# Performance work log

Hardware: AMD Instinct MI355X
Metric: run time of the kernel (lower is better)

## Reference

```python
import jax, jax.numpy as jnp
import numpy as np

B, T, D = 2, 2048, 1024
H, RANK = 16, 16
HD = D // H  # 64


def setup_inputs() -> dict:
    key = jax.random.key(0)
    ks = jax.random.split(key, 10)
    x = jax.random.normal(ks[0], (B, T, D), dtype=jnp.float32)
    def lin(k):
        kw, kb = jax.random.split(k)
        W = jax.random.normal(kw, (D, D), dtype=jnp.float32) * (1.0 / np.sqrt(D))
        b = jax.random.normal(kb, (D,), dtype=jnp.float32) * 0.01
        return W, b
    Wq, bq = lin(ks[1])
    Wk, bk = lin(ks[2])
    Wv, bv = lin(ks[3])
    Wo, bo = lin(ks[4])
    # per-head low-rank metric factors A_h: (min(rank, head_dim), head_dim)
    A = jax.random.normal(ks[5], (H, min(RANK, HD), HD), dtype=jnp.float32) * 0.02
    log_lambda = jnp.full((H,), jnp.log(jnp.float32(0.1)), dtype=jnp.float32)
    return {"x": x, "Wq": Wq, "bq": bq, "Wk": Wk, "bk": bk,
            "Wv": Wv, "bv": bv, "Wo": Wo, "bo": bo,
            "A": A, "log_lambda": log_lambda}


def reference(x, Wq, bq, Wk, bk, Wv, bv, Wo, bo, A, log_lambda):
    b, t, d = x.shape
    h = A.shape[0]
    hd = d // h

    def split_heads(y):
        return y.reshape(b, t, h, hd).transpose(0, 2, 1, 3)  # (b,h,t,hd)

    q = split_heads(x @ Wq.T + bq)
    k = split_heads(x @ Wk.T + bk)
    v = split_heads(x @ Wv.T + bv)

    # Metric g_h = A_h^T A_h + lam_h * I. torch.einsum('btid,dd,btjd->btj')
    # uses only diag(g) and sums over i: dist[b,t,j] = sum_d S[b,t,d]*gdiag[d]*diff[b,t,j,d]
    # where S[b,t,d] = sum_i (q[b,t,d] - k[b,i,d]) = t*q - sum_i k.
    gdiag = jnp.sum(A * A, axis=1) + jnp.exp(log_lambda)[:, None]  # (h,hd)

    ksum = jnp.sum(k, axis=2)                      # (b,h,hd)
    S = jnp.float32(t) * q - ksum[:, :, None, :]   # (b,h,t,hd)
    Sg = S * gdiag[None, :, None, :]               # (b,h,t,hd)
    c = jnp.sum(Sg * q, axis=-1)                   # (b,h,t)
    # dist_sq[b,h,t,j] = c[b,h,t] - sum_d Sg[b,h,t,d] * k[b,h,j,d]
    dist_sq = c[..., None] - jnp.einsum('bhtd,bhjd->bhtj', Sg, k)
    attn = jax.nn.softmax(-dist_sq, axis=-1)       # (b,h,t,t)
    o = jnp.einsum('bhtj,bhjd->bhtd', attn, v)     # (b,h,t,hd)
    out = o.transpose(0, 2, 1, 3).reshape(b, t, d)
    return out @ Wo.T + bo
```

## Files before the change

kernel.cpp:

```cpp
#include <hip/hip_runtime.h>
#include <math.h>

#define D_MODEL 1024
#define NHEAD   16
#define HDIM    64
#define SEQ     2048
#define BATCH   2
#define NROWS   (BATCH*SEQ)

typedef unsigned short u16;
typedef __attribute__((ext_vector_type(4))) unsigned short u16x4;
typedef __attribute__((ext_vector_type(8))) short short8;
typedef __attribute__((ext_vector_type(4))) float f32x4;
typedef __attribute__((ext_vector_type(2))) unsigned int u32x2;

#define SWZ(row, c) (((c) ^ ((row) & 7)) * 8)
#define GF(row) ((((row) + ((row) >> 2))) & 3)

__device__ __forceinline__ u16 f2bf(float x) {
    unsigned int u = __float_as_uint(x);
    u += 0x7fffu + ((u >> 16) & 1u);
    return (u16)(u >> 16);
}
__device__ __forceinline__ float bf2f(u16 h) {
    return __uint_as_float(((unsigned int)h) << 16);
}
__device__ __forceinline__ unsigned int cvt_pk_bf16(float a, float b) {
    unsigned int r;
    asm("v_cvt_pk_bf16_f32 %0, %1, %2" : "=v"(r) : "v"(a), "v"(b));
    return r;
}
__device__ __forceinline__ void st8(u16* p, short8 v) {
    u16x4 a, b;
    a[0]=(u16)v[0]; a[1]=(u16)v[1]; a[2]=(u16)v[2]; a[3]=(u16)v[3];
    b[0]=(u16)v[4]; b[1]=(u16)v[5]; b[2]=(u16)v[6]; b[3]=(u16)v[7];
    *(u16x4*)p = a; *(u16x4*)(p + 4) = b;
}
__device__ __forceinline__ void gld16(const u16* g, u16* l) {
    __builtin_amdgcn_global_load_lds(
        (const __attribute__((address_space(1))) void*)g,
        (__attribute__((address_space(3))) void*)l, 16, 0, 0);
}

__device__ __forceinline__ void xcd_decode(int bid, int& member, int& g) {
    const int xcd = bid & 7;
    const int rest = bid >> 3;
    member = rest & 15;
    g = ((rest >> 4) << 3) | xcd;
}

__global__ void gdiag_kernel(const float* __restrict__ A,
                             const float* __restrict__ log_lambda,
                             float* __restrict__ gdiag) {
    int id = blockIdx.x * 256 + threadIdx.x;
    if (id >= NHEAD * HDIM) return;
    int h = id >> 6, d = id & 63;
    float s = 0.f;
#pragma unroll
    for (int i = 0; i < 16; ++i) {
        float a = A[(h * 16 + i) * HDIM + d];
        s += a * a;
    }
    gdiag[id] = (s + __expf(log_lambda[h])) * 1.4426950408889634f;
}

__global__ void prep_split(const float* __restrict__ x,
                           const float* __restrict__ Wq, const float* __restrict__ Wk,
                           const float* __restrict__ Wv, const float* __restrict__ Wo,
                           u16* __restrict__ xh, u16* __restrict__ xl,
                           u16* __restrict__ wqh, u16* __restrict__ wql,
                           u16* __restrict__ wkh, u16* __restrict__ wkl,
                           u16* __restrict__ wvh, u16* __restrict__ woh) {
    int seg = blockIdx.y;
    int i = blockIdx.x * 256 + threadIdx.x;
    const float* src; u16* dh; u16* dl; int n4;
    if      (seg == 0) { src = x;  dh = xh;  dl = xl;      n4 = NROWS * D_MODEL / 4; }
    else if (seg == 1) { src = Wq; dh = wqh; dl = wql;     n4 = D_MODEL * D_MODEL / 4; }
    else if (seg == 2) { src = Wk; dh = wkh; dl = wkl;     n4 = D_MODEL * D_MODEL / 4; }
    else if (seg == 3) { src = Wv; dh = wvh; dl = nullptr; n4 = D_MODEL * D_MODEL / 4; }
    else               { src = Wo; dh = woh; dl = nullptr; n4 = D_MODEL * D_MODEL / 4; }
    if (i >= n4) return;
    float4 v = *(const float4*)&src[(size_t)i * 4];
    float vv[4] = {v.x, v.y, v.z, v.w};
    u16x4 hv, lv;
#pragma unroll
    for (int j = 0; j < 4; ++j) {
        u16 hb = f2bf(vv[j]);
        hv[j] = hb;
        lv[j] = f2bf(vv[j] - bf2f(hb));
    }
    *(u16x4*)&dh[(size_t)i * 4] = hv;
    if (dl) *(u16x4*)&dl[(size_t)i * 4] = lv;
}

template<int NP3>
__global__ __launch_bounds__(512, 4)
void gemm_mfma(const u16* __restrict__ Ah, const u16* __restrict__ Al,
               const u16* __restrict__ BhA, const u16* __restrict__ BlA, const float* __restrict__ biasA,
               float* outfA, u16* auxhA, u16* auxlA, float* ksumA,
               const u16* __restrict__ BhB, const u16* __restrict__ BlB, const float* __restrict__ biasB,
               float* outfB, u16* auxhB, u16* auxlB, float* ksumB,
               int out_layout) {
    int xtile, g;
    xcd_decode(blockIdx.x, xtile, g);
    const int ytile = g & 31;
    const int z = g >> 5;

    const u16* Bh = (z == 0) ? BhA : BhB;
    const u16* Bl = (z == 0) ? BlA : BlB;
    const float* bias = (z == 0) ? biasA : biasB;
    float* outf = (z == 0) ? outfA : outfB;
    u16* auxh   = (z == 0) ? auxhA : auxhB;
    u16* auxl   = (z == 0) ? auxlA : auxlB;
    float* ksump= (z == 0) ? ksumA : ksumB;

    __shared__ __align__(16) u16 As_h[128][32], Bs_h[64][32];
    __shared__ __align__(16) u16 As_l[NP3 ? 128 : 1][32], Bs_l[NP3 ? 64 : 1][32];

    const int tid = threadIdx.x;
    const int w = tid >> 6, lane = tid & 63, quad = lane >> 4, n16 = lane & 15;
    const int rBase = ytile * 128;
    const int cBase = xtile * 64;

    const int lrow = lane >> 2;
    const int lch  = lane & 3;
    const int arow = w * 16 + lrow;
    const int asc  = ((lch ^ GF(arow)) * 8);
    const int brow = (w & 3) * 16 + lrow;
    const int bsc  = ((lch ^ GF(brow)) * 8);

    f32x4 acc[4] = {};

    for (int kt = 0; kt < D_MODEL; kt += 32) {
        gld16(&Ah[(size_t)(rBase + arow) * D_MODEL + kt + asc], &As_h[w * 16][0]);
        if (NP3) gld16(&Al[(size_t)(rBase + arow) * D_MODEL + kt + asc], &As_l[w * 16][0]);
        if (w < 4) {
            gld16(&Bh[(size_t)(cBase + brow) * D_MODEL + kt + bsc], &Bs_h[(w & 3) * 16][0]);
        } else if (NP3) {
            gld16(&Bl[(size_t)(cBase + brow) * D_MODEL + kt + bsc], &Bs_l[NP3 ? (w & 3) * 16 : 0][0]);
        }
        __syncthreads();

        short8 a_h, a_l;
        {
            const int row = w * 16 + n16;
            const int cc = (quad ^ GF(row)) * 8;
            a_h = *(const short8*)&As_h[row][cc];
            if (NP3) a_l = *(const short8*)&As_l[NP3 ? row : 0][cc];
        }
#pragma unroll
        for (int nt = 0; nt < 4; ++nt) {
            const int row = nt * 16 + n16;
            const int cc = (quad ^ GF(row)) * 8;
            short8 b_h = *(const short8*)&Bs_h[row][cc];
            short8 b_l;
            if (NP3) b_l = *(const short8*)&Bs_l[NP3 ? row : 0][cc];
            acc[nt] = __builtin_amdgcn_mfma_f32_16x16x32_bf16(a_h, b_h, acc[nt], 0, 0, 0);
            if (NP3) {
                acc[nt] = __builtin_amdgcn_mfma_f32_16x16x32_bf16(a_h, b_l, acc[nt], 0, 0, 0);
                acc[nt] = __builtin_amdgcn_mfma_f32_16x16x32_bf16(a_l, b_h, acc[nt], 0, 0, 0);
            }
        }
        __syncthreads();
    }

    float csum[4];
#pragma unroll
    for (int nt = 0; nt < 4; ++nt) csum[nt] = 0.f;
#pragma unroll
    for (int nt = 0; nt < 4; ++nt) {
        int c = cBase + nt * 16 + n16;
        float bc = bias[c];
        int rb = rBase + w * 16 + quad * 4;
#pragma unroll
        for (int reg = 0; reg < 4; ++reg) {
            float val = acc[nt][reg] + bc;
            int rr = rb + reg;
            size_t idx = out_layout
                ? ((size_t)(((rr >> 11) * NHEAD + (c >> 6)) * SEQ + (rr & (SEQ - 1)))) * HDIM + (c & 63)
                : (size_t)rr * D_MODEL + c;
            if (outf) outf[idx] = val;
            if (auxh) {
                u16 hb = f2bf(val);
                auxh[idx] = hb;
                if (auxl) auxl[idx] = f2bf(val - bf2f(hb));
            }
            csum[nt] += val;
        }
    }
    if (ksump) {
#pragma unroll
        for (int nt = 0; nt < 4; ++nt) {
            float cs = csum[nt];
            cs += __shfl_xor(cs, 16);
            cs += __shfl_xor(cs, 32);
            if (quad == 0) {
                int c = cBase + nt * 16 + n16;
                int bb = rBase >> 11;
                atomicAdd(&ksump[(bb * NHEAD + (c >> 6)) * HDIM + (c & 63)], cs);
            }
        }
    }
}

__global__ __launch_bounds__(256)
void vtrans_kernel(const u16* __restrict__ vh, u16* __restrict__ vT) {
    __shared__ u16 tile[64][72];
    const int tid = threadIdx.x;
    const int t0 = blockIdx.x * 64;
    const int bh = blockIdx.y;
    const u16* vp = vh + (size_t)bh * SEQ * HDIM;
#pragma unroll
    for (int s = 0; s < 2; ++s) {
        int id = s * 256 + tid;
        int row = id >> 3, c8 = (id & 7) * 8;
        st8(&tile[row][c8], *(const short8*)&vp[(size_t)(t0 + row) * HDIM + c8]);
    }
    __syncthreads();
#pragma unroll
    for (int s = 0; s < 2; ++s) {
        int id = s * 256 + tid;
        int d = id >> 3, t8 = (id & 7) * 8;
        short8 r;
#pragma unroll
        for (int i = 0; i < 8; ++i) r[i] = (short)tile[t8 + i][d];
        *(short8*)&vT[((size_t)bh * HDIM + d) * SEQ + t0 + t8] = r;
    }
}

__global__ __launch_bounds__(256, 2)
void flash_mfma(const float* __restrict__ q, const u16* __restrict__ kh,
                const u16* __restrict__ kl, const u16* __restrict__ vT,
                const float* __restrict__ ksum, const float* __restrict__ gdiag,
                u16* __restrict__ o) {
    __shared__ __align__(16) u16 khs[2][64][64], kls[2][64][64], vTs[2][64][64];
    __shared__ __align__(16) u16 ps[4][32][64];

    const int tid = threadIdx.x;
    const int w = tid >> 6, lane = tid & 63, quad = lane >> 4, n16 = lane & 15;
    int qblk, g;
    xcd_decode(blockIdx.x, qblk, g);
    const int t0 = qblk * 128;
    const int h = g & 15, b = g >> 4;
    const size_t bh = (size_t)b * NHEAD + h;
    const float* qp = q + bh * SEQ * HDIM;
    const u16* khp = kh + bh * SEQ * HDIM;
    const u16* klp = kl + bh * SEQ * HDIM;
    const u16* vtp = vT + bh * HDIM * SEQ;

    short8 sgh[2][2], sgl[2][2];
#pragma unroll
    for (int mt = 0; mt < 2; ++mt) {
        int qrow = t0 + w * 32 + mt * 16 + n16;
#pragma unroll
        for (int kc = 0; kc < 2; ++kc) {
            int d0 = kc * 32 + quad * 8;
            float4 q0 = *(const float4*)&qp[(size_t)qrow * HDIM + d0];
            float4 q1 = *(const float4*)&qp[(size_t)qrow * HDIM + d0 + 4];
            float4 k0 = *(const float4*)&ksum[bh * HDIM + d0];
            float4 k1 = *(const float4*)&ksum[bh * HDIM + d0 + 4];
            float4 g0 = *(const float4*)&gdiag[(size_t)h * HDIM + d0];
            float4 g1 = *(const float4*)&gdiag[(size_t)h * HDIM + d0 + 4];
            float sg[8];
            sg[0] = (2048.f * q0.x - k0.x) * g0.x; sg[1] = (2048.f * q0.y - k0.y) * g0.y;
            sg[2] = (2048.f * q0.z - k0.z) * g0.z; sg[3] = (2048.f * q0.w - k0.w) * g0.w;
            sg[4] = (2048.f * q1.x - k1.x) * g1.x; sg[5] = (2048.f * q1.y - k1.y) * g1.y;
            sg[6] = (2048.f * q1.z - k1.z) * g1.z; sg[7] = (2048.f * q1.w - k1.w) * g1.w;
#pragma unroll
            for (int j = 0; j < 8; ++j) {
                u16 hb = f2bf(sg[j]);
                sgh[mt][kc][j] = (short)hb;
                sgl[mt][kc][j] = (short)f2bf(sg[j] - bf2f(hb));
            }
        }
    }

    f32x4 oaccv[2][4] = {};
    float m_n[2] = {-INFINITY, -INFINITY};
    float l_n[2] = {0.f, 0.f};

    const int srow = tid >> 3;
    const int sc   = tid & 7;
    const int scg  = sc * 8;
    const int scl  = SWZ(srow, sc);

    short8 rk0h = *(const short8*)&khp[(size_t)srow * HDIM + scg];
    short8 rk1h = *(const short8*)&khp[(size_t)(srow + 32) * HDIM + scg];
    short8 rk0l = *(const short8*)&klp[(size_t)srow * HDIM + scg];
    short8 rk1l = *(const short8*)&klp[(size_t)(srow + 32) * HDIM + scg];
    short8 rv0  = *(const short8*)&vtp[(size_t)srow * SEQ + scg];
    short8 rv1  = *(const short8*)&vtp[(size_t)(srow + 32) * SEQ + scg];
    *(short8*)&khs[0][srow][scl] = rk0h;  *(short8*)&khs[0][srow + 32][scl] = rk1h;
    *(short8*)&kls[0][srow][scl] = rk0l;  *(short8*)&kls[0][srow + 32][scl] = rk1l;
    *(short8*)&vTs[0][srow][scl] = rv0;   *(short8*)&vTs[0][srow + 32][scl] = rv1;

    int cur = 0;
    for (int j0 = 0; j0 < SEQ; j0 += 64, cur ^= 1) {
        __syncthreads();
        const int jn = j0 + 64;
        const bool pf = (jn < SEQ);
        if (pf) {
            rk0h = *(const short8*)&khp[(size_t)(jn + srow) * HDIM + scg];
            rk1h = *(const short8*)&khp[(size_t)(jn + srow + 32) * HDIM + scg];
            rk0l = *(const short8*)&klp[(size_t)(jn + srow) * HDIM + scg];
            rk1l = *(const short8*)&klp[(size_t)(jn + srow + 32) * HDIM + scg];
            rv0  = *(const short8*)&vtp[(size_t)srow * SEQ + jn + scg];
            rv1  = *(const short8*)&vtp[(size_t)(srow + 32) * SEQ + jn + scg];
        }

        f32x4 lgT[2][4] = {};
#pragma unroll
        for (int kc = 0; kc < 2; ++kc) {
#pragma unroll
            for (int nt = 0; nt < 4; ++nt) {
                const int row = nt * 16 + n16;
                const int cc = SWZ(row, kc * 4 + quad);
                short8 b_h = *(const short8*)&khs[cur][row][cc];
                short8 b_l = *(const short8*)&kls[cur][row][cc];
#pragma unroll
                for (int mt = 0; mt < 2; ++mt) {
                    lgT[mt][nt] = __builtin_amdgcn_mfma_f32_16x16x32_bf16(b_h, sgh[mt][kc], lgT[mt][nt], 0, 0, 0);
                    lgT[mt][nt] = __builtin_amdgcn_mfma_f32_16x16x32_bf16(b_l, sgh[mt][kc], lgT[mt][nt], 0, 0, 0);
                    lgT[mt][nt] = __builtin_amdgcn_mfma_f32_16x16x32_bf16(b_h, sgl[mt][kc], lgT[mt][nt], 0, 0, 0);
                }
            }
        }

        float mx[2];
#pragma unroll
        for (int mt = 0; mt < 2; ++mt) {
            float m0 = fmaxf(fmaxf(lgT[mt][0][0], lgT[mt][0][1]), lgT[mt][0][2]);
            m0 = fmaxf(fmaxf(m0, lgT[mt][0][3]), lgT[mt][1][0]);
            m0 = fmaxf(fmaxf(m0, lgT[mt][1][1]), lgT[mt][1][2]);
            m0 = fmaxf(fmaxf(m0, lgT[mt][1][3]), lgT[mt][2][0]);
            m0 = fmaxf(fmaxf(m0, lgT[mt][2][1]), lgT[mt][2][2]);
            m0 = fmaxf(fmaxf(m0, lgT[mt][2][3]), lgT[mt][3][0]);
            m0 = fmaxf(fmaxf(m0, lgT[mt][3][1]), lgT[mt][3][2]);
            m0 = fmaxf(m0, lgT[mt][3][3]);
            m0 = fmaxf(m0, __shfl_xor(m0, 16));
            mx[mt] = fmaxf(m0, __shfl_xor(m0, 32));
        }

        const float need = fmaxf(mx[0] - m_n[0], mx[1] - m_n[1]);
        if (!__all(need <= 8.f)) {
#pragma unroll
            for (int mt = 0; mt < 2; ++mt) {
                const float mn = fmaxf(m_n[mt], mx[mt]);
                const float alpha = exp2f(m_n[mt] - mn);
                m_n[mt] = mn;
                l_n[mt] *= alpha;
                const float a0 = __shfl(alpha, quad * 4 + 0);
                const float a1 = __shfl(alpha, quad * 4 + 1);
                const float a2 = __shfl(alpha, quad * 4 + 2);
                const float a3 = __shfl(alpha, quad * 4 + 3);
#pragma unroll
                for (int nt = 0; nt < 4; ++nt) {
                    oaccv[mt][nt][0] *= a0; oaccv[mt][nt][1] *= a1;
                    oaccv[mt][nt][2] *= a2; oaccv[mt][nt][3] *= a3;
                }
            }
        }

#pragma unroll
        for (int mt = 0; mt < 2; ++mt) {
            const int prow = mt * 16 + n16;
            const float mn = m_n[mt];
            float psum = 0.f;
#pragma unroll
            for (int nt = 0; nt < 4; ++nt) {
#pragma unroll
                for (int r = 0; r < 4; ++r) lgT[mt][nt][r] = exp2f(lgT[mt][nt][r] - mn);
                u32x2 pk;
                pk[0] = cvt_pk_bf16(lgT[mt][nt][0], lgT[mt][nt][1]);
                pk[1] = cvt_pk_bf16(lgT[mt][nt][2], lgT[mt][nt][3]);
                *(u32x2*)&ps[w][prow][SWZ(prow, nt * 2 + (quad >> 1)) + (quad & 1) * 4] = pk;
                psum += (lgT[mt][nt][0] + lgT[mt][nt][1]) + (lgT[mt][nt][2] + lgT[mt][nt][3]);
            }
            l_n[mt] += psum;
        }

        short8 pa[2][2];
#pragma unroll
        for (int mt = 0; mt < 2; ++mt) {
            const int prow = mt * 16 + n16;
            pa[mt][0] = *(const short8*)&ps[w][prow][SWZ(prow, quad)];
            pa[mt][1] = *(const short8*)&ps[w][prow][SWZ(prow, quad + 4)];
        }
#pragma unroll
        for (int nt = 0; nt < 4; ++nt) {
            const int row = nt * 16 + n16;
            short8 v0 = *(const short8*)&vTs[cur][row][SWZ(row, quad)];
            short8 v1 = *(const short8*)&vTs[cur][row][SWZ(row, quad + 4)];
#pragma unroll
            for (int mt = 0; mt < 2; ++mt) {
                oaccv[mt][nt] = __builtin_amdgcn_mfma_f32_16x16x32_bf16(pa[mt][0], v0, oaccv[mt][nt], 0, 0, 0);
                oaccv[mt][nt] = __builtin_amdgcn_mfma_f32_16x16x32_bf16(pa[mt][1], v1, oaccv[mt][nt], 0, 0, 0);
            }
        }

        if (pf) {
            const int nx = cur ^ 1;
            *(short8*)&khs[nx][srow][scl] = rk0h;  *(short8*)&khs[nx][srow + 32][scl] = rk1h;
            *(short8*)&kls[nx][srow][scl] = rk0l;  *(short8*)&kls[nx][srow + 32][scl] = rk1l;
            *(short8*)&vTs[nx][srow][scl] = rv0;   *(short8*)&vTs[nx][srow + 32][scl] = rv1;
        }
    }

#pragma unroll
    for (int mt = 0; mt < 2; ++mt) {
        float l = l_n[mt];
        l += __shfl_xor(l, 16);
        l += __shfl_xor(l, 32);
        l_n[mt] = l;
    }
#pragma unroll
    for (int mt = 0; mt < 2; ++mt) {
#pragma unroll
        for (int r = 0; r < 4; ++r) {
            float lr = __shfl(l_n[mt], quad * 4 + r);
            float inv = 1.f / lr;
            int t = t0 + w * 32 + mt * 16 + quad * 4 + r;
#pragma unroll
            for (int nt = 0; nt < 4; ++nt) {
                int d = nt * 16 + n16;
                o[((size_t)(b * SEQ + t)) * D_MODEL + h * HDIM + d] = f2bf(oaccv[mt][nt][r] * inv);
            }
        }
    }
}

extern "C" void kernel_launch(void* const* d_in, const int* in_sizes, int n_in,
                              void* d_out, int out_size, void* d_ws, size_t ws_size,
                              hipStream_t stream) {
    const float* x  = (const float*)d_in[0];
    const float* Wq = (const float*)d_in[1];
    const float* bq = (const float*)d_in[2];
    const float* Wk = (const float*)d_in[3];
    const float* bk = (const float*)d_in[4];
    const float* Wv = (const float*)d_in[5];
    const float* bv = (const float*)d_in[6];
    const float* Wo = (const float*)d_in[7];
    const float* bo = (const float*)d_in[8];
    const float* A  = (const float*)d_in[9];
    const float* ll = (const float*)d_in[10];
    float* out = (float*)d_out;

    const size_t NQKV = (size_t)NROWS * D_MODEL;
    const size_t NW = (size_t)D_MODEL * D_MODEL;
    char* base = (char*)d_ws;
    float* q_ws = (float*)base;            base += NQKV * 4;
    u16* xh  = (u16*)base;                 base += NQKV * 2;
    u16* xl  = (u16*)base;                 base += NQKV * 2;
    u16* khw = (u16*)base;                 base += NQKV * 2;
    u16* klw = (u16*)base;                 base += NQKV * 2;
    u16* vhw = (u16*)base;                 base += NQKV * 2;
    u16* wqh = (u16*)base;                 base += NW * 2;
    u16* wql = (u16*)base;                 base += NW * 2;
    u16* wkh = (u16*)base;                 base += NW * 2;
    u16* wkl = (u16*)base;                 base += NW * 2;
    u16* wvh = (u16*)base;                 base += NW * 2;
    u16* woh = (u16*)base;                 base += NW * 2;
    float* gd_ws   = (float*)base;         base += NHEAD * HDIM * 4;
    float* ksum_ws = (float*)base;         base += BATCH * NHEAD * HDIM * 4;

    hipMemsetAsync(ksum_ws, 0, BATCH * NHEAD * HDIM * sizeof(float), stream);

    prep_split<<<dim3(4096, 5), 256, 0, stream>>>(x, Wq, Wk, Wv, Wo,
                                                  xh, xl, wqh, wql, wkh, wkl, wvh, woh);
    gdiag_kernel<<<4, 256, 0, stream>>>(A, ll, gd_ws);

    gemm_mfma<1><<<1024, 512, 0, stream>>>(
        xh, xl,
        wqh, wql, bq, q_ws, nullptr, nullptr, nullptr,
        wkh, wkl, bk, nullptr, khw, klw, ksum_ws,
        1);
    gemm_mfma<0><<<512, 512, 0, stream>>>(
        xh, nullptr,
        wvh, nullptr, bv, nullptr, vhw, nullptr, nullptr,
        wvh, nullptr, bv, nullptr, vhw, nullptr, nullptr,
        1);

    u16* vTw = xl;
    u16* ohw = xh;
    vtrans_kernel<<<dim3(SEQ / 64, BATCH * NHEAD), 256, 0, stream>>>(vhw, vTw);

    flash_mfma<<<512, 256, 0, stream>>>(
        q_ws, khw, klw, vTw, ksum_ws, gd_ws, ohw);

    gemm_mfma<0><<<512, 512, 0, stream>>>(
        ohw, nullptr,
        woh, nullptr, bo, out, nullptr, nullptr, nullptr,
        woh, nullptr, bo, out, nullptr, nullptr, nullptr,
        0);
}
```

Baseline: 297.0 us.

## Software-pipeline QK MFMA of next tile with softmax/PV of previous tile

Restructures the flash attention loop so the QK^T MFMAs for tile j are issued alongside the softmax and PV for tile j-1, letting MFMA work overlap with exp and LDS traffic. V gets a triple-buffered LDS slot because it is consumed one iteration later than K. This costs more registers for the carried logits (lgP) and more LDS, which may put the two-blocks-per-CU occupancy target at risk or cause spills.

```diff
diff --git a/kernel.cpp b/kernel.cpp
--- a/kernel.cpp
+++ b/kernel.cpp
@@ -228,12 +228,113 @@
     }
 }
 
+__device__ __forceinline__ void qk_mfma(f32x4 (&lg)[2][4],
+                                        const u16 (*kh)[64], const u16 (*kl)[64],
+                                        const short8 (&sgh)[2][2], const short8 (&sgl)[2][2],
+                                        int quad, int n16) {
+#pragma unroll
+    for (int mt = 0; mt < 2; ++mt)
+#pragma unroll
+        for (int nt = 0; nt < 4; ++nt) lg[mt][nt] = (f32x4){0.f, 0.f, 0.f, 0.f};
+#pragma unroll
+    for (int kc = 0; kc < 2; ++kc) {
+#pragma unroll
+        for (int nt = 0; nt < 4; ++nt) {
+            const int row = nt * 16 + n16;
+            const int cc = SWZ(row, kc * 4 + quad);
+            short8 b_h = *(const short8*)&kh[row][cc];
+            short8 b_l = *(const short8*)&kl[row][cc];
+#pragma unroll
+            for (int mt = 0; mt < 2; ++mt) {
+                lg[mt][nt] = __builtin_amdgcn_mfma_f32_16x16x32_bf16(b_h, sgh[mt][kc], lg[mt][nt], 0, 0, 0);
+                lg[mt][nt] = __builtin_amdgcn_mfma_f32_16x16x32_bf16(b_l, sgh[mt][kc], lg[mt][nt], 0, 0, 0);
+                lg[mt][nt] = __builtin_amdgcn_mfma_f32_16x16x32_bf16(b_h, sgl[mt][kc], lg[mt][nt], 0, 0, 0);
+            }
+        }
+    }
+}
+
+__device__ __forceinline__ void softmax_pv(f32x4 (&lg)[2][4], float (&m_n)[2], float (&l_n)[2],
+                                           f32x4 (&oaccv)[2][4],
+                                           u16 (*psw)[64],
+                                           const u16 (*vt)[64],
+                                           int quad, int n16) {
+    float mx[2];
+#pragma unroll
+    for (int mt = 0; mt < 2; ++mt) {
+        float m0 = fmaxf(fmaxf(lg[mt][0][0], lg[mt][0][1]), lg[mt][0][2]);
+        m0 = fmaxf(fmaxf(m0, lg[mt][0][3]), lg[mt][1][0]);
+        m0 = fmaxf(fmaxf(m0, lg[mt][1][1]), lg[mt][1][2]);
+        m0 = fmaxf(fmaxf(m0, lg[mt][1][3]), lg[mt][2][0]);
+        m0 = fmaxf(fmaxf(m0, lg[mt][2][1]), lg[mt][2][2]);
+        m0 = fmaxf(fmaxf(m0, lg[mt][2][3]), lg[mt][3][0]);
+        m0 = fmaxf(fmaxf(m0, lg[mt][3][1]), lg[mt][3][2]);
+        m0 = fmaxf(m0, lg[mt][3][3]);
+        m0 = fmaxf(m0, __shfl_xor(m0, 16));
+        mx[mt] = fmaxf(m0, __shfl_xor(m0, 32));
+    }
+    const float need = fmaxf(mx[0] - m_n[0], mx[1] - m_n[1]);
+    if (!__all(need <= 8.f)) {
+#pragma unroll
+        for (int mt = 0; mt < 2; ++mt) {
+            const float mn = fmaxf(m_n[mt], mx[mt]);
+            const float alpha = exp2f(m_n[mt] - mn);
+            m_n[mt] = mn;
+            l_n[mt] *= alpha;
+            const float a0 = __shfl(alpha, quad * 4 + 0);
+            const float a1 = __shfl(alpha, quad * 4 + 1);
+            const float a2 = __shfl(alpha, quad * 4 + 2);
+            const float a3 = __shfl(alpha, quad * 4 + 3);
+#pragma unroll
+            for (int nt = 0; nt < 4; ++nt) {
+                oaccv[mt][nt][0] *= a0; oaccv[mt][nt][1] *= a1;
+                oaccv[mt][nt][2] *= a2; oaccv[mt][nt][3] *= a3;
+            }
+        }
+    }
+#pragma unroll
+    for (int mt = 0; mt < 2; ++mt) {
+        const int prow = mt * 16 + n16;
+        const float mn = m_n[mt];
+        float psum = 0.f;
+#pragma unroll
+        for (int nt = 0; nt < 4; ++nt) {
+#pragma unroll
+            for (int r = 0; r < 4; ++r) lg[mt][nt][r] = exp2f(lg[mt][nt][r] - mn);
+            u32x2 pk;
+            pk[0] = cvt_pk_bf16(lg[mt][nt][0], lg[mt][nt][1]);
+            pk[1] = cvt_pk_bf16(lg[mt][nt][2], lg[mt][nt][3]);
+            *(u32x2*)&psw[prow][SWZ(prow, nt * 2 + (quad >> 1)) + (quad & 1) * 4] = pk;
+            psum += (lg[mt][nt][0] + lg[mt][nt][1]) + (lg[mt][nt][2] + lg[mt][nt][3]);
+        }
+        l_n[mt] += psum;
+    }
+    short8 pa[2][2];
+#pragma unroll
+    for (int mt = 0; mt < 2; ++mt) {
+        const int prow = mt * 16 + n16;
+        pa[mt][0] = *(const short8*)&psw[prow][SWZ(prow, quad)];
+        pa[mt][1] = *(const short8*)&psw[prow][SWZ(prow, quad + 4)];
+    }
+#pragma unroll
+    for (int nt = 0; nt < 4; ++nt) {
+        const int row = nt * 16 + n16;
+        short8 v0 = *(const short8*)&vt[row][SWZ(row, quad)];
+        short8 v1 = *(const short8*)&vt[row][SWZ(row, quad + 4)];
+#pragma unroll
+        for (int mt = 0; mt < 2; ++mt) {
+            oaccv[mt][nt] = __builtin_amdgcn_mfma_f32_16x16x32_bf16(pa[mt][0], v0, oaccv[mt][nt], 0, 0, 0);
+            oaccv[mt][nt] = __builtin_amdgcn_mfma_f32_16x16x32_bf16(pa[mt][1], v1, oaccv[mt][nt], 0, 0, 0);
+        }
+    }
+}
+
 __global__ __launch_bounds__(256, 2)
 void flash_mfma(const float* __restrict__ q, const u16* __restrict__ kh,
                 const u16* __restrict__ kl, const u16* __restrict__ vT,
                 const float* __restrict__ ksum, const float* __restrict__ gdiag,
                 u16* __restrict__ o) {
-    __shared__ __align__(16) u16 khs[2][64][64], kls[2][64][64], vTs[2][64][64];
+    __shared__ __align__(16) u16 khs[2][64][64], kls[2][64][64], vTs[3][64][64];
     __shared__ __align__(16) u16 ps[4][32][64];
 
     const int tid = threadIdx.x;
@@ -276,6 +377,7 @@
     }
 
     f32x4 oaccv[2][4] = {};
+    f32x4 lgP[2][4];
     float m_n[2] = {-INFINITY, -INFINITY};
     float l_n[2] = {0.f, 0.f};
 
@@ -284,22 +386,36 @@
     const int scg  = sc * 8;
     const int scl  = SWZ(srow, sc);
 
-    short8 rk0h = *(const short8*)&khp[(size_t)srow * HDIM + scg];
-    short8 rk1h = *(const short8*)&khp[(size_t)(srow + 32) * HDIM + scg];
-    short8 rk0l = *(const short8*)&klp[(size_t)srow * HDIM + scg];
-    short8 rk1l = *(const short8*)&klp[(size_t)(srow + 32) * HDIM + scg];
-    short8 rv0  = *(const short8*)&vtp[(size_t)srow * SEQ + scg];
-    short8 rv1  = *(const short8*)&vtp[(size_t)(srow + 32) * SEQ + scg];
-    *(short8*)&khs[0][srow][scl] = rk0h;  *(short8*)&khs[0][srow + 32][scl] = rk1h;
-    *(short8*)&kls[0][srow][scl] = rk0l;  *(short8*)&kls[0][srow + 32][scl] = rk1l;
-    *(short8*)&vTs[0][srow][scl] = rv0;   *(short8*)&vTs[0][srow + 32][scl] = rv1;
-
-    int cur = 0;
-    for (int j0 = 0; j0 < SEQ; j0 += 64, cur ^= 1) {
+    const int NT = SEQ / 64;
+
+    *(short8*)&khs[0][srow][scl]      = *(const short8*)&khp[(size_t)srow * HDIM + scg];
+    *(short8*)&khs[0][srow + 32][scl] = *(const short8*)&khp[(size_t)(srow + 32) * HDIM + scg];
+    *(short8*)&kls[0][srow][scl]      = *(const short8*)&klp[(size_t)srow * HDIM + scg];
+    *(short8*)&kls[0][srow + 32][scl] = *(const short8*)&klp[(size_t)(srow + 32) * HDIM + scg];
+    *(short8*)&vTs[0][srow][scl]      = *(const short8*)&vtp[(size_t)srow * SEQ + scg];
+    *(short8*)&vTs[0][srow + 32][scl] = *(const short8*)&vtp[(size_t)(srow + 32) * SEQ + scg];
+    __syncthreads();
+
+    qk_mfma(lgP, khs[0], kls[0], sgh, sgl, quad, n16);
+    {
+        const int j0 = 64;
+        *(short8*)&khs[1][srow][scl]      = *(const short8*)&khp[(size_t)(j0 + srow) * HDIM + scg];
+        *(short8*)&khs[1][srow + 32][scl] = *(const short8*)&khp[(size_t)(j0 + srow + 32) * HDIM + scg];
+        *(short8*)&kls[1][srow][scl]      = *(const short8*)&klp[(size_t)(j0 + srow) * HDIM + scg];
+        *(short8*)&kls[1][srow + 32][scl] = *(const short8*)&klp[(size_t)(j0 + srow + 32) * HDIM + scg];
+        *(short8*)&vTs[1][srow][scl]      = *(const short8*)&vtp[(size_t)srow * SEQ + j0 + scg];
+        *(short8*)&vTs[1][srow + 32][scl] = *(const short8*)&vtp[(size_t)(srow + 32) * SEQ + j0 + scg];
+    }
+
+    for (int j = 1; j < NT; ++j) {
         __syncthreads();
-        const int jn = j0 + 64;
-        const bool pf = (jn < SEQ);
+        const int kcur = j & 1;
+        const int vprev = (j - 1) % 3;
+        const bool pf = (j + 1 < NT);
+
+        short8 rk0h, rk1h, rk0l, rk1l, rv0, rv1;
         if (pf) {
+            const int jn = (j + 1) * 64;
             rk0h = *(const short8*)&khp[(size_t)(jn + srow) * HDIM + scg];
             rk1h = *(const short8*)&khp[(size_t)(jn + srow + 32) * HDIM + scg];
             rk0l = *(const short8*)&klp[(size_t)(jn + srow) * HDIM + scg];
@@ -308,103 +424,25 @@
             rv1  = *(const short8*)&vtp[(size_t)(srow + 32) * SEQ + jn + scg];
         }
 
-        f32x4 lgT[2][4] = {};
-#pragma unroll
-        for (int kc = 0; kc < 2; ++kc) {
-#pragma unroll
-            for (int nt = 0; nt < 4; ++nt) {
-                const int row = nt * 16 + n16;
-                const int cc = SWZ(row, kc * 4 + quad);
-                short8 b_h = *(const short8*)&khs[cur][row][cc];
-                short8 b_l = *(const short8*)&kls[cur][row][cc];
-#pragma unroll
-                for (int mt = 0; mt < 2; ++mt) {
-                    lgT[mt][nt] = __builtin_amdgcn_mfma_f32_16x16x32_bf16(b_h, sgh[mt][kc], lgT[mt][nt], 0, 0, 0);
-                    lgT[mt][nt] = __builtin_amdgcn_mfma_f32_16x16x32_bf16(b_l, sgh[mt][kc], lgT[mt][nt], 0, 0, 0);
-                    lgT[mt][nt] = __builtin_amdgcn_mfma_f32_16x16x32_bf16(b_h, sgl[mt][kc], lgT[mt][nt], 0, 0, 0);
-                }
-            }
-        }
-
-        float mx[2];
-#pragma unroll
-        for (int mt = 0; mt < 2; ++mt) {
-            float m0 = fmaxf(fmaxf(lgT[mt][0][0], lgT[mt][0][1]), lgT[mt][0][2]);
-            m0 = fmaxf(fmaxf(m0, lgT[mt][0][3]), lgT[mt][1][0]);
-            m0 = fmaxf(fmaxf(m0, lgT[mt][1][1]), lgT[mt][1][2]);
-            m0 = fmaxf(fmaxf(m0, lgT[mt][1][3]), lgT[mt][2][0]);
-            m0 = fmaxf(fmaxf(m0, lgT[mt][2][1]), lgT[mt][2][2]);
-            m0 = fmaxf(fmaxf(m0, lgT[mt][2][3]), lgT[mt][3][0]);
-            m0 = fmaxf(fmaxf(m0, lgT[mt][3][1]), lgT[mt][3][2]);
-            m0 = fmaxf(m0, lgT[mt][3][3]);
-            m0 = fmaxf(m0, __shfl_xor(m0, 16));
-            mx[mt] = fmaxf(m0, __shfl_xor(m0, 32));
-        }
-
-        const float need = fmaxf(mx[0] - m_n[0], mx[1] - m_n[1]);
-        if (!__all(need <= 8.f)) {
-#pragma unroll
-            for (int mt = 0; mt < 2; ++mt) {
-                const float mn = fmaxf(m_n[mt], mx[mt]);
-                const float alpha = exp2f(m_n[mt] - mn);
-                m_n[mt] = mn;
-                l_n[mt] *= alpha;
-                const float a0 = __shfl(alpha, quad * 4 + 0);
-                const float a1 = __shfl(alpha, quad * 4 + 1);
-                const float a2 = __shfl(alpha, quad * 4 + 2);
-                const float a3 = __shfl(alpha, quad * 4 + 3);
-#pragma unroll
-                for (int nt = 0; nt < 4; ++nt) {
-                    oaccv[mt][nt][0] *= a0; oaccv[mt][nt][1] *= a1;
-                    oaccv[mt][nt][2] *= a2; oaccv[mt][nt][3] *= a3;
-                }
-            }
-        }
-
-#pragma unroll
-        for (int mt = 0; mt < 2; ++mt) {
-            const int prow = mt * 16 + n16;
-            const float mn = m_n[mt];
-            float psum = 0.f;
-#pragma unroll
-            for (int nt = 0; nt < 4; ++nt) {
-#pragma unroll
-                for (int r = 0; r < 4; ++r) lgT[mt][nt][r] = exp2f(lgT[mt][nt][r] - mn);
-                u32x2 pk;
-                pk[0] = cvt_pk_bf16(lgT[mt][nt][0], lgT[mt][nt][1]);
-                pk[1] = cvt_pk_bf16(lgT[mt][nt][2], lgT[mt][nt][3]);
-                *(u32x2*)&ps[w][prow][SWZ(prow, nt * 2 + (quad >> 1)) + (quad & 1) * 4] = pk;
-                psum += (lgT[mt][nt][0] + lgT[mt][nt][1]) + (lgT[mt][nt][2] + lgT[mt][nt][3]);
-            }
-            l_n[mt] += psum;
-        }
-
-        short8 pa[2][2];
-#pragma unroll
-        for (int mt = 0; mt < 2; ++mt) {
-            const int prow = mt * 16 + n16;
-            pa[mt][0] = *(const short8*)&ps[w][prow][SWZ(prow, quad)];
-            pa[mt][1] = *(const short8*)&ps[w][prow][SWZ(prow, quad + 4)];
-        }
-#pragma unroll
-        for (int nt = 0; nt < 4; ++nt) {
-            const int row = nt * 16 + n16;
-            short8 v0 = *(const short8*)&vTs[cur][row][SWZ(row, quad)];
-            short8 v1 = *(const short8*)&vTs[cur][row][SWZ(row, quad + 4)];
-#pragma unroll
-            for (int mt = 0; mt < 2; ++mt) {
-                oaccv[mt][nt] = __builtin_amdgcn_mfma_f32_16x16x32_bf16(pa[mt][0], v0, oaccv[mt][nt], 0, 0, 0);
-                oaccv[mt][nt] = __builtin_amdgcn_mfma_f32_16x16x32_bf16(pa[mt][1], v1, oaccv[mt][nt], 0, 0, 0);
-            }
-        }
+        f32x4 lgC[2][4];
+        qk_mfma(lgC, khs[kcur], kls[kcur], sgh, sgl, quad, n16);
+        softmax_pv(lgP, m_n, l_n, oaccv, ps[w], vTs[vprev], quad, n16);
 
         if (pf) {
-            const int nx = cur ^ 1;
-            *(short8*)&khs[nx][srow][scl] = rk0h;  *(short8*)&khs[nx][srow + 32][scl] = rk1h;
-            *(short8*)&kls[nx][srow][scl] = rk0l;  *(short8*)&kls[nx][srow + 32][scl] = rk1l;
-            *(short8*)&vTs[nx][srow][scl] = rv0;   *(short8*)&vTs[nx][srow + 32][scl] = rv1;
-        }
-    }
+            const int kn = (j + 1) & 1;
+            const int vn = (j + 1) % 3;
+            *(short8*)&khs[kn][srow][scl] = rk0h;  *(short8*)&khs[kn][srow + 32][scl] = rk1h;
+            *(short8*)&kls[kn][srow][scl] = rk0l;  *(short8*)&kls[kn][srow + 32][scl] = rk1l;
+            *(short8*)&vTs[vn][srow][scl] = rv0;   *(short8*)&vTs[vn][srow + 32][scl] = rv1;
+        }
+
+#pragma unroll
+        for (int mt = 0; mt < 2; ++mt)
+#pragma unroll
+            for (int nt = 0; nt < 4; ++nt) lgP[mt][nt] = lgC[mt][nt];
+    }
+
+    softmax_pv(lgP, m_n, l_n, oaccv, ps[w], vTs[(NT - 1) % 3], quad, n16);
 
 #pragma unroll
     for (int mt = 0; mt < 2; ++mt) {
```

New measurement: 298.5 us. Within noise of the previous version (+0.5%).
